# Performance work log

Hardware: AMD Instinct MI355X
Metric: run time of the kernel (lower is better)

Reference implementation:

```python
import jax, jax.numpy as jnp
import numpy as np

N_DFT = 512
N_FILTER = N_DFT // 2 + 1  # 257
N_HOP = N_DFT // 2         # 256
AMIN = 1e-10
DYNAMIC_RANGE = 80.0


def _dft_kernels(n_dft):
    """Windowed real-DFT kernels, shape (n_dft, n_filter) each."""
    n_filter = n_dft // 2 + 1
    n = np.arange(n_dft)
    # periodic Hann (scipy.signal.hann(n_dft, sym=False))
    win = 0.5 - 0.5 * np.cos(2.0 * np.pi * n / n_dft)
    ang = 2.0 * np.pi * np.outer(n, np.arange(n_filter)) / n_dft  # (n_dft, n_filter)
    k_real = (np.cos(ang) * win[:, None]).astype(np.float32)
    k_imag = (np.sin(ang) * win[:, None]).astype(np.float32)
    return jnp.asarray(k_real), jnp.asarray(k_imag)


def setup_inputs() -> dict:
    key = jax.random.key(0)
    x = jax.random.normal(key, (32, 2, 262144), dtype=jnp.float32)  # (batch, ch, samples)
    k_real, k_imag = _dft_kernels(N_DFT)
    return {"x": x, "k_real": k_real, "k_imag": k_imag}


def reference(x, k_real, k_imag):
    n_dft = k_real.shape[0]
    n_hop = n_dft // 2
    B, C, L = x.shape
    # TF/Keras 'same' padding with stride n_hop
    n_frame = -(-L // n_hop)
    rem = L % n_hop
    pad_total = max(n_dft - n_hop, 0) if rem == 0 else max(n_dft - rem, 0)
    pad_l = pad_total // 2
    xp = jnp.pad(x, ((0, 0), (0, 0), (pad_l, pad_total - pad_l)))
    # frame the signal: (B, C, n_frame, n_dft)
    idx = jnp.arange(n_frame)[:, None] * n_hop + jnp.arange(n_dft)[None, :]
    frames = xp[:, :, idx]
    # DFT via dense GEMM with cos/sin kernels
    re = jnp.einsum('bctd,df->bctf', frames, k_real)
    im = jnp.einsum('bctd,df->bctf', frames, k_imag)
    power = re * re + im * im  # (B, C, n_frame, n_filter)
    # channels_last output: (B, n_freq, n_time, n_ch)
    out = jnp.transpose(power, (0, 3, 2, 1))
    # power_spectrogram == 2.0 -> no pow adjustment; decibel conversion:
    log10 = jnp.float32(np.log(10.0))
    log_spec = 10.0 * jnp.log(jnp.maximum(out, AMIN)) / log10
    log_spec = log_spec - jnp.max(log_spec)
    return jnp.maximum(log_spec, -DYNAMIC_RANGE)
```

## Files before the change

kernel.cpp:

```cpp
#include <hip/hip_runtime.h>
#include <math.h>

#define L_IN     262144
#define N_FRAME  1024
#define AMIN     1e-10f
#define DRANGE   80.0f
#define UNITS_CH 1056
#define WS_HI_OFF   4096
#define WS_HALF     524288

typedef short bf16x8 __attribute__((ext_vector_type(8)));
typedef float f32x16 __attribute__((ext_vector_type(16)));

__device__ __forceinline__ short f2bf(float f) {
    unsigned u = __float_as_uint(f);
    u = (u + 0x7FFFu + ((u >> 16) & 1u)) >> 16;
    return (short)u;
}
__device__ __forceinline__ float bf2f(short h) {
    return __uint_as_float(((unsigned)(unsigned short)h) << 16);
}
__device__ __forceinline__ int swz(int u) { return u ^ ((u >> 5) & 7); }

__global__ __launch_bounds__(256) void wconv_kernel(
    const float* __restrict__ kr, const float* __restrict__ ki,
    short* __restrict__ whi, short* __restrict__ wlo, unsigned* __restrict__ wsmax)
{
    if (blockIdx.x == 0 && threadIdx.x == 0) wsmax[0] = 0u;
    const int tid  = threadIdx.x;
    const int pair = blockIdx.x * 4 + (tid >> 6);
    const int lane = tid & 63;
    const int fi = pair >> 5, kk = pair & 31;
    const int g = fi >> 1, nf = fi & 1;
    const int n  = lane & 31;
    const int k0 = kk * 16 + (lane >> 5) * 8;
    const int f  = g * 32 + n;
    bf16x8 h8, l8;
    #pragma unroll
    for (int j = 0; j < 8; ++j) {
        const int k = k0 + j;
        float w;
        if (nf == 1 && g == 0 && n == 0) w = kr[k * 257 + 256];
        else                             w = (nf ? ki : kr)[k * 257 + f];
        short hh = f2bf(w);
        h8[j] = hh;
        l8[j] = f2bf(w - bf2f(hh));
    }
    const int off = ((fi * 32 + kk) * 64 + lane) * 8;
    *(bf16x8*)(whi + off) = h8;
    *(bf16x8*)(wlo + off) = l8;
}

__global__ __launch_bounds__(512) void spec_kernel(
    const float* __restrict__ x,
    const short* __restrict__ whi, const short* __restrict__ wlo,
    float* __restrict__ out, unsigned* __restrict__ wsmax)
{
    __shared__ short Ah[2 * UNITS_CH * 8];
    __shared__ short Al[2 * UNITS_CH * 8];
    __shared__ float wmax[8];

    const int blk = blockIdx.x;
    const int tt  = blk & 31;
    const int b   = blk >> 5;
    const int tid = threadIdx.x;
    const int lane = tid & 63;
    const int g    = tid >> 6;
    const int col  = lane & 31;
    const int half = lane >> 5;

    const int s_origin = tt * 8192 - 128;
    const bool interior = (tt > 0) && (tt < 31);
    for (int U = tid; U < 2 * UNITS_CH; U += 512) {
        const int ch = (U >= UNITS_CH) ? 1 : 0;
        const int u  = U - ch * UNITS_CH;
        const int g0 = s_origin + u * 8;
        const float* xp = x + ((size_t)b * 2 + ch) * L_IN;
        float v[8];
        if (interior) {
            float4 p0 = *(const float4*)(xp + g0);
            float4 p1 = *(const float4*)(xp + g0 + 4);
            v[0]=p0.x; v[1]=p0.y; v[2]=p0.z; v[3]=p0.w;
            v[4]=p1.x; v[5]=p1.y; v[6]=p1.z; v[7]=p1.w;
        } else {
            #pragma unroll
            for (int j = 0; j < 8; ++j) {
                const int idx = g0 + j;
                v[j] = (idx >= 0 && idx < L_IN) ? xp[idx] : 0.0f;
            }
        }
        bf16x8 h8, l8;
        #pragma unroll
        for (int j = 0; j < 8; ++j) {
            short hh = f2bf(v[j]);
            h8[j] = hh;
            l8[j] = f2bf(v[j] - bf2f(hh));
        }
        const int su = swz(u);
        *(bf16x8*)&Ah[(ch * UNITS_CH + su) * 8] = h8;
        *(bf16x8*)&Al[(ch * UNITS_CH + su) * 8] = l8;
    }
    __syncthreads();

    f32x16 acc[2][2];
    #pragma unroll
    for (int mf = 0; mf < 2; ++mf)
        #pragma unroll
        for (int nf = 0; nf < 2; ++nf)
            #pragma unroll
            for (int r = 0; r < 16; ++r) acc[mf][nf][r] = 0.0f;

    const int laneoff = lane * 8;
    bf16x8 bh[2][2], bl[2][2];
    #pragma unroll
    for (int nf = 0; nf < 2; ++nf)
        #pragma unroll
        for (int kh = 0; kh < 2; ++kh) {
            const int off = (((g * 2 + nf) * 32 + kh) * 64) * 8 + laneoff;
            bh[nf][kh] = *(const bf16x8*)(whi + off);
            bl[nf][kh] = *(const bf16x8*)(wlo + off);
        }

    for (int kp = 0; kp < 16; ++kp) {
        bf16x8 ah[2][2], al[2][2];
        #pragma unroll
        for (int mf = 0; mf < 2; ++mf)
            #pragma unroll
            for (int kh = 0; kh < 2; ++kh) {
                const int u = col * 32 + kp * 4 + kh * 2 + half;
                const int e = (mf * UNITS_CH + swz(u)) * 8;
                ah[mf][kh] = *(const bf16x8*)&Ah[e];
                al[mf][kh] = *(const bf16x8*)&Al[e];
            }
        bf16x8 nbh[2][2], nbl[2][2];
        if (kp < 15) {
            #pragma unroll
            for (int nf = 0; nf < 2; ++nf)
                #pragma unroll
                for (int kh = 0; kh < 2; ++kh) {
                    const int off = (((g * 2 + nf) * 32 + (kp + 1) * 2 + kh) * 64) * 8 + laneoff;
                    nbh[nf][kh] = *(const bf16x8*)(whi + off);
                    nbl[nf][kh] = *(const bf16x8*)(wlo + off);
                }
        }
        #pragma unroll
        for (int kh = 0; kh < 2; ++kh)
            #pragma unroll
            for (int mf = 0; mf < 2; ++mf)
                #pragma unroll
                for (int nf = 0; nf < 2; ++nf)
                    acc[mf][nf] = __builtin_amdgcn_mfma_f32_32x32x16_bf16(ah[mf][kh], bh[nf][kh], acc[mf][nf], 0, 0, 0);
        #pragma unroll
        for (int kh = 0; kh < 2; ++kh)
            #pragma unroll
            for (int mf = 0; mf < 2; ++mf)
                #pragma unroll
                for (int nf = 0; nf < 2; ++nf)
                    acc[mf][nf] = __builtin_amdgcn_mfma_f32_32x32x16_bf16(al[mf][kh], bh[nf][kh], acc[mf][nf], 0, 0, 0);
        #pragma unroll
        for (int kh = 0; kh < 2; ++kh)
            #pragma unroll
            for (int mf = 0; mf < 2; ++mf)
                #pragma unroll
                for (int nf = 0; nf < 2; ++nf)
                    acc[mf][nf] = __builtin_amdgcn_mfma_f32_32x32x16_bf16(ah[mf][kh], bl[nf][kh], acc[mf][nf], 0, 0, 0);
        #pragma unroll
        for (int nf = 0; nf < 2; ++nf)
            #pragma unroll
            for (int kh = 0; kh < 2; ++kh) {
                bh[nf][kh] = nbh[nf][kh]; bl[nf][kh] = nbl[nf][kh];
            }
    }

    const bool nyq = (g == 0) && (col == 0);
    float pmax = 0.0f;
    #pragma unroll
    for (int mf = 0; mf < 2; ++mf) {
        const int f = g * 32 + col;
        #pragma unroll
        for (int r = 0; r < 16; ++r) {
            const int m = (r & 3) + 8 * (r >> 2) + 4 * half;
            const int t = tt * 32 + m;
            const float re = acc[mf][0][r];
            const float im = acc[mf][1][r];
            const float imq = nyq ? 0.0f : im;
            float p = fmaxf(re * re + imq * imq, AMIN);
            pmax = fmaxf(pmax, p);
            out[(((size_t)b * 257 + f) * N_FRAME + t) * 2 + mf] = p;
            if (nyq) {
                float pn = fmaxf(im * im, AMIN);
                pmax = fmaxf(pmax, pn);
                out[(((size_t)b * 257 + 256) * N_FRAME + t) * 2 + mf] = pn;
            }
        }
    }

    #pragma unroll
    for (int off = 32; off > 0; off >>= 1)
        pmax = fmaxf(pmax, __shfl_down(pmax, off, 64));
    if (lane == 0) wmax[g] = pmax;
    __syncthreads();
    if (tid == 0) {
        float m2 = wmax[0];
        #pragma unroll
        for (int w = 1; w < 8; ++w) m2 = fmaxf(m2, wmax[w]);
        atomicMax(wsmax, __float_as_uint(m2));
    }
}

__global__ __launch_bounds__(256) void finalize_kernel(
    float* __restrict__ out, const unsigned* __restrict__ ws_max, int n4)
{
    const int i = blockIdx.x * 256 + threadIdx.x;
    if (i >= n4) return;
    const float mlog = 10.0f * log10f(__uint_as_float(*ws_max));
    float4 p = ((const float4*)out)[i];
    float4 v;
    v.x = fmaxf(10.0f * log10f(p.x) - mlog, -DRANGE);
    v.y = fmaxf(10.0f * log10f(p.y) - mlog, -DRANGE);
    v.z = fmaxf(10.0f * log10f(p.z) - mlog, -DRANGE);
    v.w = fmaxf(10.0f * log10f(p.w) - mlog, -DRANGE);
    ((float4*)out)[i] = v;
}

extern "C" void kernel_launch(void* const* d_in, const int* in_sizes, int n_in,
                              void* d_out, int out_size, void* d_ws, size_t ws_size,
                              hipStream_t stream) {
    const float* x  = (const float*)d_in[0];
    const float* kr = (const float*)d_in[1];
    const float* ki = (const float*)d_in[2];
    float* out      = (float*)d_out;

    unsigned* wsmax = (unsigned*)d_ws;
    short* whi      = (short*)((char*)d_ws + WS_HI_OFF);
    short* wlo      = (short*)((char*)d_ws + WS_HI_OFF + WS_HALF);

    wconv_kernel<<<128, 256, 0, stream>>>(kr, ki, whi, wlo, wsmax);

    const int nblocks = 32 * 32;
    spec_kernel<<<nblocks, 512, 0, stream>>>(x, whi, wlo, out, wsmax);

    const int n4 = out_size / 4;
    finalize_kernel<<<(n4 + 255) / 256, 256, 0, stream>>>(out, wsmax, n4);
}
```

Measured before the change: 239.8 us.

## Stage output through LDS for coalesced stores and coalesce input loads

```diff
diff --git a/kernel.cpp b/kernel.cpp
--- a/kernel.cpp
+++ b/kernel.cpp
@@ -8,8 +8,10 @@
 #define UNITS_CH 1056
 #define WS_HI_OFF   4096
 #define WS_HALF     524288
+#define N4_OUT   ((32 * 257 * 1024 * 2) / 4)
 
 typedef short bf16x8 __attribute__((ext_vector_type(8)));
+typedef short bf16x4 __attribute__((ext_vector_type(4)));
 typedef float f32x16 __attribute__((ext_vector_type(16)));
 
 __device__ __forceinline__ short f2bf(float f) {
@@ -51,14 +53,16 @@
     *(bf16x8*)(wlo + off) = l8;
 }
 
-__global__ __launch_bounds__(512) void spec_kernel(
+__global__ __launch_bounds__(512, 4) void spec_kernel(
     const float* __restrict__ x,
     const short* __restrict__ whi, const short* __restrict__ wlo,
     float* __restrict__ out, unsigned* __restrict__ wsmax)
 {
-    __shared__ short Ah[2 * UNITS_CH * 8];
-    __shared__ short Al[2 * UNITS_CH * 8];
+    __shared__ __align__(16) char smem[2 * 2 * UNITS_CH * 8 * sizeof(short)];
     __shared__ float wmax[8];
+    short* Ah = (short*)smem;
+    short* Al = (short*)(smem + 2 * UNITS_CH * 8 * sizeof(short));
+    float* S  = (float*)smem;
 
     const int blk = blockIdx.x;
     const int tt  = blk & 31;
@@ -70,35 +74,34 @@
     const int half = lane >> 5;
 
     const int s_origin = tt * 8192 - 128;
-    const bool interior = (tt > 0) && (tt < 31);
-    for (int U = tid; U < 2 * UNITS_CH; U += 512) {
-        const int ch = (U >= UNITS_CH) ? 1 : 0;
-        const int u  = U - ch * UNITS_CH;
-        const int g0 = s_origin + u * 8;
+    for (int cc = g; cc < 66; cc += 8) {
+        const int ch   = (cc >= 33) ? 1 : 0;
+        const int c    = cc - ch * 33;
+        const int base = s_origin + c * 256;
         const float* xp = x + ((size_t)b * 2 + ch) * L_IN;
-        float v[8];
-        if (interior) {
-            float4 p0 = *(const float4*)(xp + g0);
-            float4 p1 = *(const float4*)(xp + g0 + 4);
-            v[0]=p0.x; v[1]=p0.y; v[2]=p0.z; v[3]=p0.w;
-            v[4]=p1.x; v[5]=p1.y; v[6]=p1.z; v[7]=p1.w;
+        const int i4 = base + lane * 4;
+        float v[4];
+        if (base >= 0 && base + 256 <= L_IN) {
+            float4 p = *(const float4*)(xp + i4);
+            v[0] = p.x; v[1] = p.y; v[2] = p.z; v[3] = p.w;
         } else {
             #pragma unroll
-            for (int j = 0; j < 8; ++j) {
-                const int idx = g0 + j;
+            for (int j = 0; j < 4; ++j) {
+                const int idx = i4 + j;
                 v[j] = (idx >= 0 && idx < L_IN) ? xp[idx] : 0.0f;
             }
         }
-        bf16x8 h8, l8;
-        #pragma unroll
-        for (int j = 0; j < 8; ++j) {
+        bf16x4 h4, l4;
+        #pragma unroll
+        for (int j = 0; j < 4; ++j) {
             short hh = f2bf(v[j]);
-            h8[j] = hh;
-            l8[j] = f2bf(v[j] - bf2f(hh));
-        }
-        const int su = swz(u);
-        *(bf16x8*)&Ah[(ch * UNITS_CH + su) * 8] = h8;
-        *(bf16x8*)&Al[(ch * UNITS_CH + su) * 8] = l8;
+            h4[j] = hh;
+            l4[j] = f2bf(v[j] - bf2f(hh));
+        }
+        const int u = c * 32 + (lane >> 1);
+        const int e = (ch * UNITS_CH + swz(u)) * 8 + (lane & 1) * 4;
+        *(bf16x4*)&Ah[e] = h4;
+        *(bf16x4*)&Al[e] = l4;
     }
     __syncthreads();
 
@@ -121,6 +124,7 @@
             bl[nf][kh] = *(const bf16x8*)(wlo + off);
         }
 
+    #pragma unroll 2
     for (int kp = 0; kp < 16; ++kp) {
         bf16x8 ah[2][2], al[2][2];
         #pragma unroll
@@ -172,29 +176,27 @@
             }
     }
 
+    __syncthreads();
     const bool nyq = (g == 0) && (col == 0);
     float pmax = 0.0f;
     #pragma unroll
     for (int mf = 0; mf < 2; ++mf) {
-        const int f = g * 32 + col;
         #pragma unroll
         for (int r = 0; r < 16; ++r) {
             const int m = (r & 3) + 8 * (r >> 2) + 4 * half;
-            const int t = tt * 32 + m;
             const float re = acc[mf][0][r];
             const float im = acc[mf][1][r];
             const float imq = nyq ? 0.0f : im;
             float p = fmaxf(re * re + imq * imq, AMIN);
             pmax = fmaxf(pmax, p);
-            out[(((size_t)b * 257 + f) * N_FRAME + t) * 2 + mf] = p;
+            S[(m * 2 + mf) * 257 + g * 32 + col] = p;
             if (nyq) {
                 float pn = fmaxf(im * im, AMIN);
                 pmax = fmaxf(pmax, pn);
-                out[(((size_t)b * 257 + 256) * N_FRAME + t) * 2 + mf] = pn;
-            }
-        }
-    }
-
+                S[(m * 2 + mf) * 257 + 256] = pn;
+            }
+        }
+    }
     #pragma unroll
     for (int off = 32; off > 0; off >>= 1)
         pmax = fmaxf(pmax, __shfl_down(pmax, off, 64));
@@ -205,6 +207,16 @@
         #pragma unroll
         for (int w = 1; w < 8; ++w) m2 = fmaxf(m2, wmax[w]);
         atomicMax(wsmax, __float_as_uint(m2));
+    }
+    float* obase = out + (size_t)b * 526336 + (size_t)tt * 64;
+    for (int q = tid; q < 257 * 16; q += 512) {
+        const int f = q >> 4, part = q & 15;
+        float4 vv;
+        vv.x = S[(part * 4 + 0) * 257 + f];
+        vv.y = S[(part * 4 + 1) * 257 + f];
+        vv.z = S[(part * 4 + 2) * 257 + f];
+        vv.w = S[(part * 4 + 3) * 257 + f];
+        *(float4*)(obase + (size_t)f * 2048 + part * 4) = vv;
     }
 }
 
@@ -240,6 +252,6 @@
     const int nblocks = 32 * 32;
     spec_kernel<<<nblocks, 512, 0, stream>>>(x, whi, wlo, out, wsmax);
 
-    const int n4 = out_size / 4;
+    const int n4 = N4_OUT;
     finalize_kernel<<<(n4 + 255) / 256, 256, 0, stream>>>(out, wsmax, n4);
 }
```

Result: slower. 548.4 us (+128.6%).
